# Performance work log

Hardware: AMD Instinct MI355X
Metric: run time of the kernel (lower is better)

The kernel has to match this reference:

```python
import jax, jax.numpy as jnp
import numpy as np
from jax import lax

NEG_SLOPE = 0.2
BN_EPS = 1e-5


def _edges(n_nodes, n_total):
    # complete graph (no self loops) on the first n_nodes nodes, as in create_complete_graph,
    # plus PyG GATConv default add_self_loops over ALL n_total nodes.
    i = np.arange(n_nodes)
    src = np.repeat(i, n_nodes)
    dst = np.tile(i, n_nodes)
    keep = src != dst
    loops = np.arange(n_total)
    src = np.concatenate([src[keep], loops]).astype(np.int32)
    dst = np.concatenate([dst[keep], loops]).astype(np.int32)
    return jnp.asarray(src), jnp.asarray(dst)


def _bn_eval(x, g, b, m, v):
    # x: [B, C, H, W]; eval-mode batchnorm with running stats
    inv = g / jnp.sqrt(v + BN_EPS)
    return x * inv[None, :, None, None] + (b - m * inv)[None, :, None, None]


def _gat(x, W, a_src, a_dst, bias, src, dst, n_total):
    h = x @ W                      # [N, D_out]
    s = h @ a_src                  # [N] per-node source score
    d = h @ a_dst                  # [N] per-node dest score
    e = jax.nn.leaky_relu(s[src] + d[dst], NEG_SLOPE)          # [E]
    emax = jax.ops.segment_max(e, dst, num_segments=n_total)   # [N]
    ex = jnp.exp(e - emax[dst])
    denom = jax.ops.segment_sum(ex, dst, num_segments=n_total)
    alpha = ex / denom[dst]                                    # [E]
    out = jax.ops.segment_sum(alpha[:, None] * h[src], dst, num_segments=n_total)
    return out + bias


def setup_inputs() -> dict:
    key = jax.random.key(0)
    ks = jax.random.split(key, 12)
    B, H, W = 8, 64, 64

    def rn(k, shape, s):
        return jax.random.normal(k, shape, jnp.float32) * s

    return {
        "images": jax.random.normal(ks[0], (B, 3, H, W), jnp.float32),
        "conv1_w": rn(ks[1], (64, 3, 3, 3), 0.1), "conv1_b": jnp.zeros((64,), jnp.float32),
        "bn1_g": jnp.ones((64,), jnp.float32), "bn1_b": jnp.zeros((64,), jnp.float32),
        "bn1_m": jnp.zeros((64,), jnp.float32), "bn1_v": jnp.ones((64,), jnp.float32),
        "conv2_w": rn(ks[2], (128, 64, 3, 3), 0.05), "conv2_b": jnp.zeros((128,), jnp.float32),
        "bn2_g": jnp.ones((128,), jnp.float32), "bn2_b": jnp.zeros((128,), jnp.float32),
        "bn2_m": jnp.zeros((128,), jnp.float32), "bn2_v": jnp.ones((128,), jnp.float32),
        "gat1_w": rn(ks[3], (128, 256), 0.05), "gat1_asrc": rn(ks[4], (256,), 0.05),
        "gat1_adst": rn(ks[5], (256,), 0.05), "gat1_bias": jnp.zeros((256,), jnp.float32),
        "gat2_w": rn(ks[6], (256, 128), 0.05), "gat2_asrc": rn(ks[7], (128,), 0.05),
        "gat2_adst": rn(ks[8], (128,), 0.05), "gat2_bias": jnp.zeros((128,), jnp.float32),
        "out_w": rn(ks[9], (128, 10), 0.05), "out_b": jnp.zeros((10,), jnp.float32),
    }


def reference(images, conv1_w, conv1_b, bn1_g, bn1_b, bn1_m, bn1_v,
              conv2_w, conv2_b, bn2_g, bn2_b, bn2_m, bn2_v,
              gat1_w, gat1_asrc, gat1_adst, gat1_bias,
              gat2_w, gat2_asrc, gat2_adst, gat2_bias,
              out_w, out_b):
    dn = ("NCHW", "OIHW", "NCHW")
    x = lax.conv_general_dilated(images, conv1_w, (1, 1), "SAME", dimension_numbers=dn)
    x = x + conv1_b[None, :, None, None]
    x = jax.nn.relu(_bn_eval(x, bn1_g, bn1_b, bn1_m, bn1_v))
    x = lax.reduce_window(x, -jnp.inf, lax.max, (1, 1, 2, 2), (1, 1, 2, 2), "VALID")
    x = lax.conv_general_dilated(x, conv2_w, (1, 1), "SAME", dimension_numbers=dn)
    x = x + conv2_b[None, :, None, None]
    x = jax.nn.relu(_bn_eval(x, bn2_g, bn2_b, bn2_m, bn2_v))

    B = x.shape[0]
    n_nodes = x.shape[2] * x.shape[3]          # (H/2)*(W/2) = 1024
    x = x.reshape(B, 128, n_nodes).transpose(0, 2, 1).reshape(-1, 128)  # [B*n, 128]
    n_total = B * n_nodes
    src, dst = _edges(n_nodes, n_total)

    x = jax.nn.relu(_gat(x, gat1_w, gat1_asrc, gat1_adst, gat1_bias, src, dst, n_total))
    x = jax.nn.relu(_gat(x, gat2_w, gat2_asrc, gat2_adst, gat2_bias, src, dst, n_total))

    x = x.reshape(B, n_nodes, 128).mean(axis=1)   # global_mean_pool over each image's nodes
    logits = x @ out_w + out_b
    return jax.nn.log_softmax(logits, axis=1)
```

## Files before the change

### kernel.cpp

```cpp
#include <hip/hip_runtime.h>
#include <math.h>

#define BN_EPS 1e-5f
#define NEG_SLOPE 0.2f

__device__ __forceinline__ float relu_f(float x) { return x > 0.f ? x : 0.f; }
__device__ __forceinline__ float leaky_f(float z) { return z > 0.f ? z : NEG_SLOPE * z; }

__global__ void conv1_pool(const float* __restrict__ img, const float* __restrict__ w,
                           const float* __restrict__ cb, const float* __restrict__ g,
                           const float* __restrict__ bb, const float* __restrict__ m,
                           const float* __restrict__ vv, float* __restrict__ out)
{
    int blk = blockIdx.x;
    int q = blk & 3, cog = (blk >> 2) & 15, b = blk >> 6;
    int t = threadIdx.x;
    int x = t & 31, y = (q << 3) + (t >> 5);

    float acc[4][4] = {};
#pragma unroll
    for (int ci = 0; ci < 3; ++ci) {
        const float* ib = img + (b * 3 + ci) * 4096;
        float rv[4][4];
#pragma unroll
        for (int r = 0; r < 4; ++r) {
            int yy = 2 * y - 1 + r;
            bool yok = (unsigned)yy < 64u;
            const float* p = ib + yy * 64 + 2 * x;
            float2 c01 = yok ? *(const float2*)p : make_float2(0.f, 0.f);
            rv[r][1] = c01.x;
            rv[r][2] = c01.y;
            rv[r][0] = (yok && x > 0) ? p[-1] : 0.f;
            rv[r][3] = (yok && x < 31) ? p[2] : 0.f;
        }
#pragma unroll
        for (int j = 0; j < 4; ++j) {
            const float* wj = w + ((cog * 4 + j) * 3 + ci) * 9;
#pragma unroll
            for (int ky = 0; ky < 3; ++ky)
#pragma unroll
                for (int kx = 0; kx < 3; ++kx) {
                    float wvv = wj[ky * 3 + kx];
#pragma unroll
                    for (int py = 0; py < 2; ++py)
#pragma unroll
                        for (int px = 0; px < 2; ++px)
                            acc[j][py * 2 + px] += rv[py + ky][px + kx] * wvv;
                }
        }
    }
#pragma unroll
    for (int j = 0; j < 4; ++j) {
        int co = cog * 4 + j;
        float inv = g[co] / sqrtf(vv[co] + BN_EPS);
        float sh = cb[co] * inv + (bb[co] - m[co] * inv);
        float v0 = relu_f(acc[j][0] * inv + sh);
        float v1 = relu_f(acc[j][1] * inv + sh);
        float v2 = relu_f(acc[j][2] * inv + sh);
        float v3 = relu_f(acc[j][3] * inv + sh);
        out[((b * 64 + co) * 32 + y) * 32 + x] = fmaxf(fmaxf(v0, v1), fmaxf(v2, v3));
    }
}

__device__ __forceinline__ void c2load(const float* cbase, int y, int x4, bool xl, bool xr,
                                       float r6[3][6])
{
#pragma unroll
    for (int r = 0; r < 3; ++r) {
        int yy = y - 1 + r;
        bool yok = (unsigned)yy < 32u;
        const float* p = cbase + yy * 32 + x4;
        float4 f = yok ? *(const float4*)p : make_float4(0.f, 0.f, 0.f, 0.f);
        r6[r][1] = f.x; r6[r][2] = f.y; r6[r][3] = f.z; r6[r][4] = f.w;
        r6[r][0] = (yok && xl) ? p[-1] : 0.f;
        r6[r][5] = (yok && xr) ? p[4] : 0.f;
    }
}

__global__ void conv2_fused(const float* __restrict__ in, const float* __restrict__ w,
                            const float* __restrict__ cb, const float* __restrict__ g,
                            const float* __restrict__ bb, const float* __restrict__ m,
                            const float* __restrict__ vv, float* __restrict__ x0)
{
    int blk = blockIdx.x;
    int half = blk & 1, cog = (blk >> 1) & 31, b = blk >> 6;
    int t = threadIdx.x;
    int x4 = (t & 7) * 4;
    int y = half * 16 + (t >> 3);
    bool xl = x4 > 0, xr = x4 < 28;
    const float* ibase = in + b * 64 * 1024;

    float rc[3][6], rn[3][6];
    c2load(ibase, y, x4, xl, xr, rc);

    float acc[4][4] = {};
    for (int ci = 0; ci < 64; ++ci) {
        if (ci < 63) c2load(ibase + (ci + 1) * 1024, y, x4, xl, xr, rn);
#pragma unroll
        for (int j = 0; j < 4; ++j) {
            const float* wj = w + ((cog * 4 + j) * 64 + ci) * 9;
#pragma unroll
            for (int ky = 0; ky < 3; ++ky)
#pragma unroll
                for (int kx = 0; kx < 3; ++kx) {
                    float wvv = wj[ky * 3 + kx];
#pragma unroll
                    for (int p = 0; p < 4; ++p)
                        acc[j][p] += rc[ky][p + kx] * wvv;
                }
        }
#pragma unroll
        for (int r = 0; r < 3; ++r)
#pragma unroll
            for (int k = 0; k < 6; ++k) rc[r][k] = rn[r][k];
    }

#pragma unroll
    for (int j = 0; j < 4; ++j) {
        int co = cog * 4 + j;
        float inv = g[co] / sqrtf(vv[co] + BN_EPS);
        float sh = cb[co] * inv + (bb[co] - m[co] * inv);
#pragma unroll
        for (int p = 0; p < 4; ++p) {
            int n = b * 1024 + y * 32 + x4 + p;
            x0[(size_t)n * 128 + co] = relu_f(acc[j][p] * inv + sh);
        }
    }
}

template <int K, int N>
__global__ void gemm_tiled(const float* __restrict__ A, const float* __restrict__ B,
                           float* __restrict__ C)
{
    __shared__ float As[16][64];
    __shared__ float Bs[16][64];
    int t = threadIdx.x;
    int m0 = blockIdx.x * 64;
    int n0 = blockIdx.y * 64;
    int tx = t & 15, ty = t >> 4;
    int am = t >> 2, akq = (t & 3) * 4;
    int bk = t >> 4, bn = (t & 15) * 4;
    float acc[4][4] = {};

    for (int k0 = 0; k0 < K; k0 += 16) {
        float4 av = *(const float4*)&A[(size_t)(m0 + am) * K + k0 + akq];
        float4 bv = *(const float4*)&B[(size_t)(k0 + bk) * N + n0 + bn];
        __syncthreads();
        As[akq + 0][am] = av.x;
        As[akq + 1][am] = av.y;
        As[akq + 2][am] = av.z;
        As[akq + 3][am] = av.w;
        *(float4*)&Bs[bk][bn] = bv;
        __syncthreads();
#pragma unroll
        for (int kk = 0; kk < 16; ++kk) {
            float4 a4 = *(const float4*)&As[kk][ty * 4];
            float4 b4 = *(const float4*)&Bs[kk][tx * 4];
            float aa[4] = {a4.x, a4.y, a4.z, a4.w};
            float bb4[4] = {b4.x, b4.y, b4.z, b4.w};
#pragma unroll
            for (int i = 0; i < 4; ++i)
#pragma unroll
                for (int j = 0; j < 4; ++j)
                    acc[i][j] += aa[i] * bb4[j];
        }
    }
#pragma unroll
    for (int i = 0; i < 4; ++i) {
        float4 o = {acc[i][0], acc[i][1], acc[i][2], acc[i][3]};
        *(float4*)&C[(size_t)(m0 + ty * 4 + i) * N + n0 + tx * 4] = o;
    }
}

__global__ void score_kernel(const float* __restrict__ h, const float* __restrict__ asrc,
                             const float* __restrict__ adst, float* __restrict__ s,
                             float* __restrict__ d, int D, int N)
{
    int gt = blockIdx.x * blockDim.x + threadIdx.x;
    int wave = gt >> 6, lane = gt & 63;
    if (wave >= N) return;
    const float* hp = h + (size_t)wave * D;
    float ss = 0.f, dd = 0.f;
    for (int c = lane; c < D; c += 64) {
        float hv = hp[c];
        ss += hv * asrc[c];
        dd += hv * adst[c];
    }
    for (int off = 32; off; off >>= 1) {
        ss += __shfl_down(ss, off);
        dd += __shfl_down(dd, off);
    }
    if (lane == 0) { s[wave] = ss; d[wave] = dd; }
}

template <int D, int KS>
__global__ void gat_agg_gemm(const float* __restrict__ h, const float* __restrict__ s,
                             const float* __restrict__ d, float* __restrict__ pacc,
                             float* __restrict__ pden)
{
    __shared__ float Ss[1024];
    __shared__ float As[16][64];
    __shared__ float Bs[16][64];
    __shared__ float red[4];
    __shared__ float part[16][64];

    const int CH = 1024 / KS;
    int t = threadIdx.x;
    int m0 = blockIdx.x * 64;
    int n0 = blockIdx.y * 64;
    int kz = blockIdx.z;
    int tx = t & 15, ty = t >> 4;
    int av4 = tx * 4;

    float4 s4 = *(const float4*)&s[t * 4];
    *(float4*)&Ss[t * 4] = s4;
    float lm = fmaxf(fmaxf(s4.x, s4.y), fmaxf(s4.z, s4.w));
#pragma unroll
    for (int off = 1; off < 64; off <<= 1) lm = fmaxf(lm, __shfl_xor(lm, off));
    if ((t & 63) == 0) red[t >> 6] = lm;
    __syncthreads();
    float smax = fmaxf(fmaxf(red[0], red[1]), fmaxf(red[2], red[3]));

    float4 dv = *(const float4*)&d[m0 + av4];
    float4 mv = {leaky_f(smax + dv.x), leaky_f(smax + dv.y),
                 leaky_f(smax + dv.z), leaky_f(smax + dv.w)};
    float4 dsum = {0.f, 0.f, 0.f, 0.f};
    float acc[4][4] = {};

    for (int k0 = kz * CH; k0 < kz * CH + CH; k0 += 16) {
        float4 bv = *(const float4*)&h[(size_t)(k0 + ty) * D + n0 + tx * 4];
        float su = Ss[k0 + ty];
        float4 avv;
        avv.x = __expf(leaky_f(su + dv.x) - mv.x);
        avv.y = __expf(leaky_f(su + dv.y) - mv.y);
        avv.z = __expf(leaky_f(su + dv.z) - mv.z);
        avv.w = __expf(leaky_f(su + dv.w) - mv.w);
        dsum.x += avv.x; dsum.y += avv.y; dsum.z += avv.z; dsum.w += avv.w;
        __syncthreads();
        *(float4*)&As[ty][av4] = avv;
        *(float4*)&Bs[ty][tx * 4] = bv;
        __syncthreads();
#pragma unroll
        for (int kk = 0; kk < 16; ++kk) {
            float4 a4 = *(const float4*)&As[kk][ty * 4];
            float4 b4 = *(const float4*)&Bs[kk][tx * 4];
            float aa[4] = {a4.x, a4.y, a4.z, a4.w};
            float bb4[4] = {b4.x, b4.y, b4.z, b4.w};
#pragma unroll
            for (int i = 0; i < 4; ++i)
#pragma unroll
                for (int j = 0; j < 4; ++j)
                    acc[i][j] += aa[i] * bb4[j];
        }
    }

    __syncthreads();
    *(float4*)&part[ty][av4] = dsum;
    __syncthreads();

#pragma unroll
    for (int i = 0; i < 4; ++i) {
        int r = ty * 4 + i;
        float4 o = {acc[i][0], acc[i][1], acc[i][2], acc[i][3]};
        *(float4*)&pacc[((size_t)kz * 1024 + m0 + r) * D + n0 + tx * 4] = o;
    }
    if (t < 64) {
        float den = 0.f;
#pragma unroll
        for (int u = 0; u < 16; ++u) den += part[u][t];
        pden[kz * 1024 + m0 + t] = den;
    }
}

template <int D, int KS>
__global__ void gat_combine(const float* __restrict__ pacc, const float* __restrict__ pden,
                            const float* __restrict__ bias, float* __restrict__ out)
{
    int idx = blockIdx.x * blockDim.x + threadIdx.x;
    if (idx >= 1024 * D / 4) return;
    int c4 = idx & (D / 4 - 1);
    int v = idx / (D / 4);
    float4 a = {0.f, 0.f, 0.f, 0.f};
    float den = 0.f;
#pragma unroll
    for (int ks = 0; ks < KS; ++ks) {
        float4 p = ((const float4*)pacc)[(size_t)(ks * 1024 + v) * (D / 4) + c4];
        a.x += p.x; a.y += p.y; a.z += p.z; a.w += p.w;
        den += pden[ks * 1024 + v];
    }
    float rd = 1.f / den;
    float4 bz = ((const float4*)bias)[c4];
    float4 o = {relu_f(a.x * rd + bz.x), relu_f(a.y * rd + bz.y),
                relu_f(a.z * rd + bz.z), relu_f(a.w * rd + bz.w)};
    ((float4*)out)[(size_t)v * (D / 4) + c4] = o;
}

template <int D>
__global__ void gat_self4(const float* __restrict__ h, const float* __restrict__ bias,
                          float* __restrict__ out)
{
    int idx = blockIdx.x * blockDim.x + threadIdx.x;
    if (idx >= 7168 * D / 4) return;
    int c4 = idx & (D / 4 - 1);
    int n = 1024 + idx / (D / 4);
    float4 v = ((const float4*)h)[(size_t)n * (D / 4) + c4];
    float4 bz = ((const float4*)bias)[c4];
    float4 o = {relu_f(v.x + bz.x), relu_f(v.y + bz.y),
                relu_f(v.z + bz.z), relu_f(v.w + bz.w)};
    ((float4*)out)[(size_t)n * (D / 4) + c4] = o;
}

__global__ void pool_part(const float* __restrict__ x2, float* __restrict__ part)
{
    int b = blockIdx.x >> 4, seg = blockIdx.x & 15, t = threadIdx.x;
    const float* p = x2 + ((size_t)b * 1024 + seg * 64) * 128 + t;
    float acc = 0.f;
#pragma unroll 8
    for (int n = 0; n < 64; ++n) acc += p[(size_t)n * 128];
    part[(b * 16 + seg) * 128 + t] = acc;
}

__global__ void head_kernel(const float* __restrict__ part, const float* __restrict__ ow,
                            const float* __restrict__ ob, float* __restrict__ out)
{
    __shared__ float pooled[128];
    __shared__ float logits[10];
    int b = blockIdx.x, t = threadIdx.x;
    float acc = 0.f;
#pragma unroll
    for (int sgi = 0; sgi < 16; ++sgi) acc += part[(b * 16 + sgi) * 128 + t];
    pooled[t] = acc * (1.f / 1024.f);
    __syncthreads();
    if (t < 10) {
        float l = ob[t];
        for (int c = 0; c < 128; ++c) l += pooled[c] * ow[c * 10 + t];
        logits[t] = l;
    }
    __syncthreads();
    if (t == 0) {
        float mx = logits[0];
        for (int j = 1; j < 10; ++j) mx = fmaxf(mx, logits[j]);
        float sum = 0.f;
        for (int j = 0; j < 10; ++j) sum += expf(logits[j] - mx);
        float lse = mx + logf(sum);
        for (int j = 0; j < 10; ++j) out[b * 10 + j] = logits[j] - lse;
    }
}

extern "C" void kernel_launch(void* const* d_in, const int* in_sizes, int n_in,
                              void* d_out, int out_size, void* d_ws, size_t ws_size,
                              hipStream_t stream)
{
    const float* images = (const float*)d_in[0];
    const float* c1w = (const float*)d_in[1];
    const float* c1b = (const float*)d_in[2];
    const float* bn1g = (const float*)d_in[3];
    const float* bn1b = (const float*)d_in[4];
    const float* bn1m = (const float*)d_in[5];
    const float* bn1v = (const float*)d_in[6];
    const float* c2w = (const float*)d_in[7];
    const float* c2b = (const float*)d_in[8];
    const float* bn2g = (const float*)d_in[9];
    const float* bn2b = (const float*)d_in[10];
    const float* bn2m = (const float*)d_in[11];
    const float* bn2v = (const float*)d_in[12];
    const float* g1w = (const float*)d_in[13];
    const float* g1as = (const float*)d_in[14];
    const float* g1ad = (const float*)d_in[15];
    const float* g1b = (const float*)d_in[16];
    const float* g2w = (const float*)d_in[17];
    const float* g2as = (const float*)d_in[18];
    const float* g2ad = (const float*)d_in[19];
    const float* g2b = (const float*)d_in[20];
    const float* ow = (const float*)d_in[21];
    const float* ob = (const float*)d_in[22];
    float* out = (float*)d_out;

    float* ws = (float*)d_ws;
    float* x1    = ws;
    float* buf2  = ws + 2097152;
    float* x0    = ws + 2621440;
    float* h1    = ws + 3670016;
    float* s1    = ws + 5767168;
    float* d1    = ws + 5775360;
    float* h2    = ws + 5783552;
    float* s2    = ws + 6832128;
    float* d2    = ws + 6840320;
    float* part  = buf2;
    float* pden1 = buf2 + 32768;
    float* pden2 = buf2 + 49152;
    float* pacc1 = x0;
    float* pacc2 = x1;
    float* x2 = x0;

    conv1_pool<<<512, 256, 0, stream>>>(images, c1w, c1b, bn1g, bn1b, bn1m, bn1v, buf2);
    conv2_fused<<<512, 128, 0, stream>>>(buf2, c2w, c2b, bn2g, bn2b, bn2m, bn2v, x0);

    gemm_tiled<128, 256><<<dim3(128, 4), 256, 0, stream>>>(x0, g1w, h1);
    score_kernel<<<256, 256, 0, stream>>>(h1, g1as, g1ad, s1, d1, 256, 1024);
    gat_agg_gemm<256, 4><<<dim3(16, 4, 4), 256, 0, stream>>>(h1, s1, d1, pacc1, pden1);
    gat_combine<256, 4><<<256, 256, 0, stream>>>(pacc1, pden1, g1b, x1);
    gat_self4<256><<<1792, 256, 0, stream>>>(h1, g1b, x1);

    gemm_tiled<256, 128><<<dim3(128, 2), 256, 0, stream>>>(x1, g2w, h2);
    score_kernel<<<256, 256, 0, stream>>>(h2, g2as, g2ad, s2, d2, 128, 1024);
    gat_agg_gemm<128, 8><<<dim3(16, 2, 8), 256, 0, stream>>>(h2, s2, d2, pacc2, pden2);
    gat_combine<128, 8><<<128, 256, 0, stream>>>(pacc2, pden2, g2b, x2);
    gat_self4<128><<<896, 256, 0, stream>>>(h2, g2b, x2);

    pool_part<<<128, 128, 0, stream>>>(x2, part);
    head_kernel<<<8, 128, 0, stream>>>(part, ow, ob, out);
}
```

Baseline: 236.1 us.

## Halve per-thread and per-block tiles in conv2, node GEMMs and GAT aggregation

conv2 now computes 2 output pixels per thread with 256 threads per block, drops the register double-buffer, and writes the 4 output channels as float4 stores. The node GEMMs and the GAT aggregation GEMM move to 32-row tiles with 128-thread blocks, and the aggregation uses a larger K-split to put more blocks in flight. The workspace layout is reorganised to fit the larger partial buffers. The aim is higher occupancy and parallelism, at the cost of more partial-sum traffic in the combine step and less register reuse per thread.

```diff
diff --git a/kernel.cpp b/kernel.cpp
--- a/kernel.cpp
+++ b/kernel.cpp
@@ -62,21 +62,6 @@
     }
 }
 
-__device__ __forceinline__ void c2load(const float* cbase, int y, int x4, bool xl, bool xr,
-                                       float r6[3][6])
-{
-#pragma unroll
-    for (int r = 0; r < 3; ++r) {
-        int yy = y - 1 + r;
-        bool yok = (unsigned)yy < 32u;
-        const float* p = cbase + yy * 32 + x4;
-        float4 f = yok ? *(const float4*)p : make_float4(0.f, 0.f, 0.f, 0.f);
-        r6[r][1] = f.x; r6[r][2] = f.y; r6[r][3] = f.z; r6[r][4] = f.w;
-        r6[r][0] = (yok && xl) ? p[-1] : 0.f;
-        r6[r][5] = (yok && xr) ? p[4] : 0.f;
-    }
-}
-
 __global__ void conv2_fused(const float* __restrict__ in, const float* __restrict__ w,
                             const float* __restrict__ cb, const float* __restrict__ g,
                             const float* __restrict__ bb, const float* __restrict__ m,
@@ -85,17 +70,31 @@
     int blk = blockIdx.x;
     int half = blk & 1, cog = (blk >> 1) & 31, b = blk >> 6;
     int t = threadIdx.x;
-    int x4 = (t & 7) * 4;
-    int y = half * 16 + (t >> 3);
-    bool xl = x4 > 0, xr = x4 < 28;
+    int x2p = (t & 15) * 2;
+    int y = half * 16 + (t >> 4);
+    bool xnz = x2p != 0;
+    bool xhi = x2p == 30;
     const float* ibase = in + b * 64 * 1024;
-
-    float rc[3][6], rn[3][6];
-    c2load(ibase, y, x4, xl, xr, rc);
-
-    float acc[4][4] = {};
+    int xb = xnz ? x2p - 1 : 0;
+
+    float acc[4][2] = {};
+
+#pragma unroll 2
     for (int ci = 0; ci < 64; ++ci) {
-        if (ci < 63) c2load(ibase + (ci + 1) * 1024, y, x4, xl, xr, rn);
+        const float* cb2 = ibase + ci * 1024;
+        float rc[3][4];
+#pragma unroll
+        for (int r = 0; r < 3; ++r) {
+            int yy = y - 1 + r;
+            bool yok = (unsigned)yy < 32u;
+            const float* p = cb2 + yy * 32 + xb;
+            float4 f = yok ? *(const float4*)p : make_float4(0.f, 0.f, 0.f, 0.f);
+            rc[r][0] = xnz ? f.x : 0.f;
+            rc[r][1] = xnz ? f.y : f.x;
+            rc[r][2] = xnz ? f.z : f.y;
+            float r3 = xnz ? f.w : f.z;
+            rc[r][3] = xhi ? 0.f : r3;
+        }
 #pragma unroll
         for (int j = 0; j < 4; ++j) {
             const float* wj = w + ((cog * 4 + j) * 64 + ci) * 9;
@@ -104,53 +103,52 @@
 #pragma unroll
                 for (int kx = 0; kx < 3; ++kx) {
                     float wvv = wj[ky * 3 + kx];
-#pragma unroll
-                    for (int p = 0; p < 4; ++p)
-                        acc[j][p] += rc[ky][p + kx] * wvv;
+                    acc[j][0] += rc[ky][kx] * wvv;
+                    acc[j][1] += rc[ky][kx + 1] * wvv;
                 }
         }
-#pragma unroll
-        for (int r = 0; r < 3; ++r)
-#pragma unroll
-            for (int k = 0; k < 6; ++k) rc[r][k] = rn[r][k];
-    }
-
+    }
+
+    float o0[4], o1[4];
 #pragma unroll
     for (int j = 0; j < 4; ++j) {
         int co = cog * 4 + j;
         float inv = g[co] / sqrtf(vv[co] + BN_EPS);
         float sh = cb[co] * inv + (bb[co] - m[co] * inv);
-#pragma unroll
-        for (int p = 0; p < 4; ++p) {
-            int n = b * 1024 + y * 32 + x4 + p;
-            x0[(size_t)n * 128 + co] = relu_f(acc[j][p] * inv + sh);
-        }
-    }
+        o0[j] = relu_f(acc[j][0] * inv + sh);
+        o1[j] = relu_f(acc[j][1] * inv + sh);
+    }
+    int n0 = b * 1024 + y * 32 + x2p;
+    float4 s0 = {o0[0], o0[1], o0[2], o0[3]};
+    float4 s1 = {o1[0], o1[1], o1[2], o1[3]};
+    *(float4*)&x0[(size_t)n0 * 128 + cog * 4] = s0;
+    *(float4*)&x0[(size_t)(n0 + 1) * 128 + cog * 4] = s1;
 }
 
 template <int K, int N>
-__global__ void gemm_tiled(const float* __restrict__ A, const float* __restrict__ B,
-                           float* __restrict__ C)
-{
-    __shared__ float As[16][64];
+__global__ void gemm32(const float* __restrict__ A, const float* __restrict__ B,
+                       float* __restrict__ C)
+{
+    __shared__ float As[16][32];
     __shared__ float Bs[16][64];
     int t = threadIdx.x;
-    int m0 = blockIdx.x * 64;
+    int m0 = blockIdx.x * 32;
     int n0 = blockIdx.y * 64;
     int tx = t & 15, ty = t >> 4;
     int am = t >> 2, akq = (t & 3) * 4;
-    int bk = t >> 4, bn = (t & 15) * 4;
     float acc[4][4] = {};
 
     for (int k0 = 0; k0 < K; k0 += 16) {
         float4 av = *(const float4*)&A[(size_t)(m0 + am) * K + k0 + akq];
-        float4 bv = *(const float4*)&B[(size_t)(k0 + bk) * N + n0 + bn];
+        float4 bv0 = *(const float4*)&B[(size_t)(k0 + ty) * N + n0 + tx * 4];
+        float4 bv1 = *(const float4*)&B[(size_t)(k0 + 8 + ty) * N + n0 + tx * 4];
         __syncthreads();
         As[akq + 0][am] = av.x;
         As[akq + 1][am] = av.y;
         As[akq + 2][am] = av.z;
         As[akq + 3][am] = av.w;
-        *(float4*)&Bs[bk][bn] = bv;
+        *(float4*)&Bs[ty][tx * 4] = bv0;
+        *(float4*)&Bs[ty + 8][tx * 4] = bv1;
         __syncthreads();
 #pragma unroll
         for (int kk = 0; kk < 16; ++kk) {
@@ -199,37 +197,41 @@
                              float* __restrict__ pden)
 {
     __shared__ float Ss[1024];
-    __shared__ float As[16][64];
+    __shared__ float As[16][32];
     __shared__ float Bs[16][64];
-    __shared__ float red[4];
-    __shared__ float part[16][64];
+    __shared__ float red[2];
+    __shared__ float part[16][32];
 
     const int CH = 1024 / KS;
     int t = threadIdx.x;
-    int m0 = blockIdx.x * 64;
+    int m0 = blockIdx.x * 32;
     int n0 = blockIdx.y * 64;
     int kz = blockIdx.z;
     int tx = t & 15, ty = t >> 4;
-    int av4 = tx * 4;
-
-    float4 s4 = *(const float4*)&s[t * 4];
-    *(float4*)&Ss[t * 4] = s4;
-    float lm = fmaxf(fmaxf(s4.x, s4.y), fmaxf(s4.z, s4.w));
+    int ug = t >> 3, vg4 = (t & 7) * 4;
+
+    float4 sa = *(const float4*)&s[t * 8];
+    float4 sb = *(const float4*)&s[t * 8 + 4];
+    *(float4*)&Ss[t * 8] = sa;
+    *(float4*)&Ss[t * 8 + 4] = sb;
+    float lm = fmaxf(fmaxf(fmaxf(sa.x, sa.y), fmaxf(sa.z, sa.w)),
+                     fmaxf(fmaxf(sb.x, sb.y), fmaxf(sb.z, sb.w)));
 #pragma unroll
     for (int off = 1; off < 64; off <<= 1) lm = fmaxf(lm, __shfl_xor(lm, off));
     if ((t & 63) == 0) red[t >> 6] = lm;
     __syncthreads();
-    float smax = fmaxf(fmaxf(red[0], red[1]), fmaxf(red[2], red[3]));
-
-    float4 dv = *(const float4*)&d[m0 + av4];
+    float smax = fmaxf(red[0], red[1]);
+
+    float4 dv = *(const float4*)&d[m0 + vg4];
     float4 mv = {leaky_f(smax + dv.x), leaky_f(smax + dv.y),
                  leaky_f(smax + dv.z), leaky_f(smax + dv.w)};
     float4 dsum = {0.f, 0.f, 0.f, 0.f};
     float acc[4][4] = {};
 
     for (int k0 = kz * CH; k0 < kz * CH + CH; k0 += 16) {
-        float4 bv = *(const float4*)&h[(size_t)(k0 + ty) * D + n0 + tx * 4];
-        float su = Ss[k0 + ty];
+        float4 bv0 = *(const float4*)&h[(size_t)(k0 + ty) * D + n0 + tx * 4];
+        float4 bv1 = *(const float4*)&h[(size_t)(k0 + 8 + ty) * D + n0 + tx * 4];
+        float su = Ss[k0 + ug];
         float4 avv;
         avv.x = __expf(leaky_f(su + dv.x) - mv.x);
         avv.y = __expf(leaky_f(su + dv.y) - mv.y);
@@ -237,8 +239,9 @@
         avv.w = __expf(leaky_f(su + dv.w) - mv.w);
         dsum.x += avv.x; dsum.y += avv.y; dsum.z += avv.z; dsum.w += avv.w;
         __syncthreads();
-        *(float4*)&As[ty][av4] = avv;
-        *(float4*)&Bs[ty][tx * 4] = bv;
+        *(float4*)&As[ug][vg4] = avv;
+        *(float4*)&Bs[ty][tx * 4] = bv0;
+        *(float4*)&Bs[ty + 8][tx * 4] = bv1;
         __syncthreads();
 #pragma unroll
         for (int kk = 0; kk < 16; ++kk) {
@@ -255,7 +258,7 @@
     }
 
     __syncthreads();
-    *(float4*)&part[ty][av4] = dsum;
+    *(float4*)&part[ug][vg4] = dsum;
     __syncthreads();
 
 #pragma unroll
@@ -264,7 +267,7 @@
         float4 o = {acc[i][0], acc[i][1], acc[i][2], acc[i][3]};
         *(float4*)&pacc[((size_t)kz * 1024 + m0 + r) * D + n0 + tx * 4] = o;
     }
-    if (t < 64) {
+    if (t < 32) {
         float den = 0.f;
 #pragma unroll
         for (int u = 0; u < 16; ++u) den += part[u][t];
@@ -378,34 +381,34 @@
 
     float* ws = (float*)d_ws;
     float* x1    = ws;
-    float* buf2  = ws + 2097152;
-    float* x0    = ws + 2621440;
-    float* h1    = ws + 3670016;
-    float* s1    = ws + 5767168;
-    float* d1    = ws + 5775360;
-    float* h2    = ws + 5783552;
-    float* s2    = ws + 6832128;
-    float* d2    = ws + 6840320;
-    float* part  = buf2;
-    float* pden1 = buf2 + 32768;
-    float* pden2 = buf2 + 49152;
+    float* bufc1 = ws + 2097152;
+    float* h1    = ws + 2621440;
+    float* x0    = ws + 4718592;
+    float* h2    = ws + 5767168;
+    float* s1    = ws + 6815744;
+    float* d1    = ws + 6816768;
+    float* s2    = ws + 6817792;
+    float* d2    = ws + 6818816;
+    float* part  = bufc1;
+    float* pden1 = bufc1 + 16384;
+    float* pden2 = bufc1 + 24576;
     float* pacc1 = x0;
-    float* pacc2 = x1;
-    float* x2 = x0;
-
-    conv1_pool<<<512, 256, 0, stream>>>(images, c1w, c1b, bn1g, bn1b, bn1m, bn1v, buf2);
-    conv2_fused<<<512, 128, 0, stream>>>(buf2, c2w, c2b, bn2g, bn2b, bn2m, bn2v, x0);
-
-    gemm_tiled<128, 256><<<dim3(128, 4), 256, 0, stream>>>(x0, g1w, h1);
+    float* pacc2 = h1;
+    float* x2    = x0;
+
+    conv1_pool<<<512, 256, 0, stream>>>(images, c1w, c1b, bn1g, bn1b, bn1m, bn1v, bufc1);
+    conv2_fused<<<512, 256, 0, stream>>>(bufc1, c2w, c2b, bn2g, bn2b, bn2m, bn2v, x0);
+
+    gemm32<128, 256><<<dim3(256, 4), 128, 0, stream>>>(x0, g1w, h1);
     score_kernel<<<256, 256, 0, stream>>>(h1, g1as, g1ad, s1, d1, 256, 1024);
-    gat_agg_gemm<256, 4><<<dim3(16, 4, 4), 256, 0, stream>>>(h1, s1, d1, pacc1, pden1);
-    gat_combine<256, 4><<<256, 256, 0, stream>>>(pacc1, pden1, g1b, x1);
+    gat_agg_gemm<256, 8><<<dim3(32, 4, 8), 128, 0, stream>>>(h1, s1, d1, pacc1, pden1);
+    gat_combine<256, 8><<<256, 256, 0, stream>>>(pacc1, pden1, g1b, x1);
     gat_self4<256><<<1792, 256, 0, stream>>>(h1, g1b, x1);
 
-    gemm_tiled<256, 128><<<dim3(128, 2), 256, 0, stream>>>(x1, g2w, h2);
+    gemm32<256, 128><<<dim3(256, 2), 128, 0, stream>>>(x1, g2w, h2);
     score_kernel<<<256, 256, 0, stream>>>(h2, g2as, g2ad, s2, d2, 128, 1024);
-    gat_agg_gemm<128, 8><<<dim3(16, 2, 8), 256, 0, stream>>>(h2, s2, d2, pacc2, pden2);
-    gat_combine<128, 8><<<128, 256, 0, stream>>>(pacc2, pden2, g2b, x2);
+    gat_agg_gemm<128, 16><<<dim3(32, 2, 16), 128, 0, stream>>>(h2, s2, d2, pacc2, pden2);
+    gat_combine<128, 16><<<128, 256, 0, stream>>>(pacc2, pden2, g2b, x2);
     gat_self4<128><<<896, 256, 0, stream>>>(h2, g2b, x2);
 
     pool_part<<<128, 128, 0, stream>>>(x2, part);
```

After: 217.4 us. -7.9%, faster.
